# Optimization experiments

Hardware: AMD Instinct MI355X
Metric: run time of the kernel (lower is better)

The kernel has to match this reference:

```python
import jax, jax.numpy as jnp
import numpy as np

B = 4096
NUM_PTS = 1000

def de_boor(knotss, t, CP, p):
    # knotss: [N, K], t: [T, N], CP: [N, ncp, 2, 1] -> [T, N, 2, 1]
    N = knotss.shape[0]
    # k[b] = number of knots in knotss[b, p+1:] strictly below t (matches torch loop)
    k = jnp.sum((t[:, :, None] > knotss[None, :, p + 1:]).astype(jnp.int32), axis=-1)  # [T, N]
    bn = jnp.arange(N)[None, :, None]
    idx = k[:, :, None] + jnp.arange(p + 1)[None, None, :]           # [T, N, p+1]
    E = CP[bn, idx]                                                  # [T, N, p+1, 2, 1]
    te = t[:, :, None, None, None]
    for j in range(1, p + 1):
        m = p - j + 1
        i = jnp.arange(m)[None, None, :]
        a1 = knotss[bn, p + 1 + i + k[:, :, None]][..., None, None]  # [T, N, m, 1, 1]
        a2 = knotss[bn, i + j + k[:, :, None]][..., None, None]
        # in torch, ascending i reads old E[i+1]; vectorized update over old E is identical
        E = ((a1 - te) * E[:, :, :m] + (te - a2) * E[:, :, 1:m + 1]) / (a1 - a2)
    return E[:, :, 0]

def first_derivative(Pc, knots):
    n = Pc.shape[1]
    den = (knots[:, 4:n + 3] - knots[:, 1:n])[:, :, None, None]
    Q = 3.0 / den * (Pc[:, 1:] - Pc[:, :-1])
    return Q, knots[:, 1:-1]

def second_derivative(Q, knots):
    n = Q.shape[1]
    den = (knots[:, 3:n + 2] - knots[:, 1:n])[:, :, None, None]
    R = 2.0 / den * (Q[:, 1:] - Q[:, :-1])
    return R, knots[:, 1:-1]

def construct(t, knots, p=3):
    # t: [B], knots: [B, K] -> N: [B, K-1]; replicates stale-tail behavior of torch loop
    K = knots.shape[1]
    N = ((t[:, None] >= knots[:, :-1]) & (t[:, None] < knots[:, 1:])).astype(knots.dtype)
    lenN = K - 2
    for power in range(1, p + 1):
        m = lenN - power
        den_a = knots[:, power:power + m] - knots[:, :m]
        a = jnp.where(den_a != 0, (t[:, None] - knots[:, :m]) / jnp.where(den_a != 0, den_a, 1.0), 0.0)
        den_b = knots[:, power + 1:power + 1 + m] - knots[:, 1:1 + m]
        b = jnp.where(den_b != 0, (knots[:, power + 1:power + 1 + m] - t[:, None]) / jnp.where(den_b != 0, den_b, 1.0), 0.0)
        N = N.at[:, :m].set(N[:, :m] * a + N[:, 1:m + 1] * b)
    return N

def construct_A(knots):
    # knots: [B, 12], 6 data points -> A: [B, 8, 8]
    Bn = knots.shape[0]
    rows = [construct(knots[:, i + 3], knots) for i in range(5)]
    # i == 5 hits the knots[0, 8] == 1 branch (clamped right end): one-hot at column 7
    row5 = jnp.zeros((Bn, knots.shape[1] - 1), knots.dtype).at[:, 7].set(1.0)
    A = jnp.stack(rows + [row5], axis=1)[:, :, :8]                   # [B, 6, 8]
    z = jnp.zeros((Bn, 1, 8), knots.dtype)
    A = jnp.concatenate([z, A, z], axis=1)                           # [B, 8, 8]
    A = A.at[:, 0, 0].add(knots[:, 5]).at[:, 0, 1].add(-knots[:, 4] - knots[:, 5]).at[:, 0, 2].add(knots[:, 4])
    A = A.at[:, -1, -3].add(1.0 - knots[:, 7]).at[:, -1, -2].add(knots[:, 7] + knots[:, 6] - 2.0).at[:, -1, -1].add(1.0 - knots[:, 6])
    return A

def solve(P, knots):
    Bn = P.shape[0]
    z = jnp.zeros((Bn, 1, 1), P.dtype)
    Px = jnp.concatenate([z, P[:, :, 0], z], axis=1)  # [B, 8, 1]
    Py = jnp.concatenate([z, P[:, :, 1], z], axis=1)
    inv = jnp.linalg.inv(construct_A(knots))
    Cx = inv @ Px
    Cy = inv @ Py
    return jnp.concatenate([Cx, Cy], axis=2)[..., None]  # [B, 8, 2, 1]

def forward(x, P, W1, b1, W2, b2, W3, b3):
    h = jax.nn.relu(x @ W1.T + b1)
    h = jax.nn.relu(h @ W2.T + b2)
    xs = jax.nn.softmax(h @ W3.T + b3, axis=1)  # [B, 5]
    # torch: w[:, i] = x[:, i] + detach(w[:, i-1]) -> cumsum in value, identity in grad
    x4 = xs[:, :4]
    w = x4 + jax.lax.stop_gradient(jnp.cumsum(x4, axis=1) - x4)
    Bn = x.shape[0]
    knots = jnp.concatenate([jnp.zeros((Bn, 4), x.dtype), w, jnp.ones((Bn, 4), x.dtype)], axis=1)  # [B, 12]
    C = solve(P, knots)  # [B, 8, 2, 1]
    # global curvature over linspace(knots[0,3]=0, knots[0,10]=1, NUM_PTS)
    L = jnp.linspace(0.0, 1.0, NUM_PTS).astype(x.dtype)
    tall = jnp.broadcast_to(L[:, None], (NUM_PTS, Bn))
    Q, dk = first_derivative(C, knots)
    R, ddk = second_derivative(Q, dk)
    sp = de_boor(dk, tall, Q, 2)    # [T, B, 2, 1] spline'
    sdp = de_boor(ddk, tall, R, 1)  # [T, B, 2, 1] spline''
    spx, spy = sp[:, :, 0, 0], sp[:, :, 1, 0]
    sdx, sdy = sdp[:, :, 0, 0], sdp[:, :, 1, 0]
    speed2 = spx ** 2 + spy ** 2
    curv = (spx * sdy - spy * sdx) / (speed2 ** 3) ** 0.5
    vals = curv ** 2 * jnp.sqrt(speed2)  # [T, B]; de_boor(knots2, J, Q, 2) == spline', reused
    S1 = vals[1::2].sum(axis=0)
    S2 = vals[0::2].sum(axis=0)
    h_step = 1.0 / (NUM_PTS - 1)
    integration = h_step / 3.0 * (4.0 * S1 + 2.0 * S2)
    return integration, knots

def setup_inputs():
    key = jax.random.key(0)
    ks = jax.random.split(key, 8)
    return {
        "x": jax.random.normal(ks[0], (B, 8), jnp.float32),
        "P": jax.random.normal(ks[1], (B, 6, 2, 1), jnp.float32),
        "W1": jax.random.normal(ks[2], (128, 8), jnp.float32) * 0.3,
        "b1": jnp.full((128,), 0.01, jnp.float32),
        "W2": jax.random.normal(ks[3], (128, 128), jnp.float32) * 0.09,
        "b2": jnp.full((128,), 0.01, jnp.float32),
        "W3": jax.random.normal(ks[4], (5, 128), jnp.float32) * 0.1,
        "b3": jnp.full((5,), 0.01, jnp.float32),
    }

def reference(x, P, W1, b1, W2, b2, W3, b3):
    return forward(x, P, W1, b1, W2, b2, W3, b3)
```

## Files before the change

kernel.cpp:

```cpp
#include <hip/hip_runtime.h>
#include <math.h>

#define BATCH 4096
#define NPTS 1000

#define WSYNC() do { asm volatile("s_waitcnt lgkmcnt(0)" ::: "memory"); \
                     __builtin_amdgcn_sched_barrier(0); } while (0)

__device__ __forceinline__ float frcp(float v) { return __builtin_amdgcn_rcpf(v); }

__global__ __launch_bounds__(256, 8) void net2_one(
    const float* __restrict__ x, const float* __restrict__ P,
    const float* __restrict__ W1, const float* __restrict__ b1,
    const float* __restrict__ W2, const float* __restrict__ b2,
    const float* __restrict__ W3, const float* __restrict__ b3,
    float* __restrict__ out_integ, float* __restrict__ out_knots)
{
    __shared__ float s_h1[8][128];
    __shared__ float s_part[4][4][5];
    __shared__ float LA[8][8][10];
    __shared__ float LQ[8][16];
    __shared__ float LR[8][16];
    __shared__ float s_coef[8][64];

    const int tid = threadIdx.x;
    const int wv = tid >> 6, lane = tid & 63;
    const int p = tid >> 7, row = tid & 127;
    const int b0 = blockIdx.x * 8;

    {
        float4 w0 = ((const float4*)(W1 + row * 8))[0];
        float4 w1 = ((const float4*)(W1 + row * 8))[1];
        float bb = b1[row];
        #pragma unroll
        for (int k = 0; k < 4; ++k) {
            const float* xr = x + (b0 + p * 4 + k) * 8;
            float4 xa = ((const float4*)xr)[0];
            float4 xb = ((const float4*)xr)[1];
            float h = bb + w0.x*xa.x + w0.y*xa.y + w0.z*xa.z + w0.w*xa.w
                         + w1.x*xb.x + w1.y*xb.y + w1.z*xb.z + w1.w*xb.w;
            s_h1[p * 4 + k][row] = fmaxf(h, 0.f);
        }
    }
    __syncthreads();

    float bb2 = b2[row];
    float a0 = bb2, a1 = bb2, a2 = bb2, a3 = bb2;
    {
        const float4* wr = (const float4*)(W2 + row * 128);
        const float4* h0 = (const float4*)s_h1[p * 4 + 0];
        const float4* h1 = (const float4*)s_h1[p * 4 + 1];
        const float4* h2p = (const float4*)s_h1[p * 4 + 2];
        const float4* h3 = (const float4*)s_h1[p * 4 + 3];
        #pragma unroll 8
        for (int c4 = 0; c4 < 32; ++c4) {
            float4 w = wr[c4];
            float4 ha = h0[c4], hb = h1[c4], hc = h2p[c4], hd = h3[c4];
            a0 += w.x*ha.x + w.y*ha.y + w.z*ha.z + w.w*ha.w;
            a1 += w.x*hb.x + w.y*hb.y + w.z*hb.z + w.w*hb.w;
            a2 += w.x*hc.x + w.y*hc.y + w.z*hc.z + w.w*hc.w;
            a3 += w.x*hd.x + w.y*hd.y + w.z*hd.z + w.w*hd.w;
        }
    }
    float h2_0 = fmaxf(a0, 0.f), h2_1 = fmaxf(a1, 0.f);
    float h2_2 = fmaxf(a2, 0.f), h2_3 = fmaxf(a3, 0.f);

    #pragma unroll
    for (int c = 0; c < 5; ++c) {
        float wc = W3[c * 128 + row];
        float p0 = wc * h2_0, p1 = wc * h2_1, p2 = wc * h2_2, p3 = wc * h2_3;
        #pragma unroll
        for (int m = 32; m >= 1; m >>= 1) {
            p0 += __shfl_xor(p0, m, 64);
            p1 += __shfl_xor(p1, m, 64);
            p2 += __shfl_xor(p2, m, 64);
            p3 += __shfl_xor(p3, m, 64);
        }
        if (lane == 0) {
            s_part[wv][0][c] = p0; s_part[wv][1][c] = p1;
            s_part[wv][2][c] = p2; s_part[wv][3][c] = p3;
        }
    }
    __syncthreads();

    if (wv == 0) {
        const int el = lane >> 3, r = lane & 7;
        const int e = b0 + el;
        const int pw = (el >> 2) * 2;

        float lg0 = s_part[pw][el & 3][0] + s_part[pw + 1][el & 3][0] + b3[0];
        float lg1 = s_part[pw][el & 3][1] + s_part[pw + 1][el & 3][1] + b3[1];
        float lg2 = s_part[pw][el & 3][2] + s_part[pw + 1][el & 3][2] + b3[2];
        float lg3 = s_part[pw][el & 3][3] + s_part[pw + 1][el & 3][3] + b3[3];
        float lg4 = s_part[pw][el & 3][4] + s_part[pw + 1][el & 3][4] + b3[4];
        float mx = fmaxf(fmaxf(fmaxf(fmaxf(lg0, lg1), lg2), lg3), lg4);
        float e0 = expf(lg0-mx), e1 = expf(lg1-mx), e2 = expf(lg2-mx),
              e3 = expf(lg3-mx), e4 = expf(lg4-mx);
        float s = e0 + e1 + e2 + e3 + e4;
        float xs0 = e0/s, xs1 = e1/s, xs2 = e2/s, xs3 = e3/s;
        float c0 = xs0, c1 = c0 + xs1, c2 = c1 + xs2, c3 = c2 + xs3;
        float w4 = xs0 + (c0 - xs0);
        float w5 = xs1 + (c1 - xs1);
        float w6 = xs2 + (c2 - xs2);
        float w7 = xs3 + (c3 - xs3);

        {
            float kv = (r < 4) ? 0.f : (r == 4 ? w4 : r == 5 ? w5 : r == 6 ? w6 : w7);
            out_knots[e * 12 + r] = kv;
            if (r < 4) {
                out_knots[e * 12 + 8 + r] = 1.f;
                s_coef[el][60 + r] = (r == 0 ? w4 : r == 1 ? w5 : r == 2 ? w6 : w7);
            }
        }

        const float ka[12] = {0.f,0.f,0.f,0.f,w4,w5,w6,w7,1.f,1.f,1.f,1.f};
        float t = (r == 2) ? w4 : (r == 3) ? w5 : (r == 4) ? w6 : (r == 5) ? w7 : 0.f;
        float N[11];
        #pragma unroll
        for (int i = 0; i < 11; ++i)
            N[i] = (t >= ka[i] && t < ka[i+1]) ? 1.f : 0.f;
        #pragma unroll
        for (int pq = 1; pq <= 3; ++pq) {
            #pragma unroll
            for (int i = 0; i < 10; ++i) {
                if (i < 10 - pq) {
                    float da = ka[i+pq] - ka[i];
                    float av = (da != 0.f) ? (t - ka[i]) * frcp(da) : 0.f;
                    float db = ka[i+pq+1] - ka[i+1];
                    float bv = (db != 0.f) ? (ka[i+pq+1] - t) * frcp(db) : 0.f;
                    N[i] = N[i] * av + N[i+1] * bv;
                }
            }
        }

        float a[10];
        #pragma unroll
        for (int c = 0; c < 8; ++c) {
            float v0 = (c==0) ? w5 : (c==1) ? (-w4-w5) : (c==2) ? w4 : 0.f;
            float v6 = (c==7) ? 1.f : 0.f;
            float v7 = (c==5) ? (1.f-w7) : (c==6) ? (w7+w6-2.f) : (c==7) ? (1.f-w6) : 0.f;
            float vb = (r==0) ? v0 : (r==6) ? v6 : v7;
            a[c] = (r >= 1 && r <= 5) ? N[c] : vb;
        }
        {
            float px = 0.f, py = 0.f;
            if (r >= 1 && r <= 6) {
                px = P[e * 12 + (r-1) * 2 + 0];
                py = P[e * 12 + (r-1) * 2 + 1];
            }
            a[8] = px; a[9] = py;
        }

        int done = 0, pcol = 7;
        #pragma unroll
        for (int col = 0; col < 8; ++col) {
            float bv = done ? -1.f : fabsf(a[col]);
            int bi = lane;
            #pragma unroll
            for (int m = 1; m <= 4; m <<= 1) {
                float ov = __shfl_xor(bv, m, 64);
                int   oi = __shfl_xor(bi, m, 64);
                if (ov > bv || (ov == bv && oi < bi)) { bv = ov; bi = oi; }
            }
            float pr[10];
            #pragma unroll
            for (int c = 0; c < 10; ++c) pr[c] = __shfl(a[c], bi, 64);
            if (lane == bi) { done = 1; pcol = col; }
            else if (!done) {
                float f = a[col] * frcp(pr[col]);
                #pragma unroll
                for (int c = 0; c < 10; ++c) if (c > col) a[c] -= f * pr[c];
            }
        }
        #pragma unroll
        for (int c = 0; c < 10; ++c) LA[el][pcol][c] = a[c];
        WSYNC();

        if (r < 2) {
            const int par = r;
            float C[8];
            #pragma unroll
            for (int col = 7; col >= 0; --col) {
                float sv = LA[el][col][8 + par];
                #pragma unroll
                for (int c = col + 1; c < 8; ++c) sv -= LA[el][col][c] * C[c];
                C[col] = sv * frcp(LA[el][col][col]);
            }
            float Qr[7], Rr[6];
            const float dq[7] = { w4, w5, w6, w7 - w4, 1.f - w5, 1.f - w6, 1.f - w7 };
            #pragma unroll
            for (int i = 0; i < 7; ++i) Qr[i] = (3.f * frcp(dq[i])) * (C[i+1] - C[i]);
            const float dr[6] = { w4, w5, w6 - w4, w7 - w5, 1.f - w6, 1.f - w7 };
            #pragma unroll
            for (int i = 0; i < 6; ++i) Rr[i] = (2.f * frcp(dr[i])) * (Qr[i+1] - Qr[i]);
            #pragma unroll
            for (int i = 0; i < 7; ++i) LQ[el][i*2+par] = Qr[i];
            #pragma unroll
            for (int i = 0; i < 6; ++i) LR[el][i*2+par] = Rr[i];
        }
        WSYNC();

        if (r < 5) {
            const int s5 = r;
            float k2 = (s5 <= 1) ? 0.f : (s5 == 2) ? w4 : (s5 == 3) ? w5 : w6;
            float k3 = (s5 == 0) ? 0.f : (s5 == 1) ? w4 : (s5 == 2) ? w5 : (s5 == 3) ? w6 : w7;
            float k4 = (s5 == 0) ? w4 : (s5 == 1) ? w5 : (s5 == 2) ? w6 : (s5 == 3) ? w7 : 1.f;
            float k5 = (s5 == 0) ? w5 : (s5 == 1) ? w6 : (s5 == 2) ? w7 : 1.f;
            float q0x = LQ[el][s5*2],     q0y = LQ[el][s5*2+1];
            float q1x = LQ[el][(s5+1)*2], q1y = LQ[el][(s5+1)*2+1];
            float q2x = LQ[el][(s5+2)*2], q2y = LQ[el][(s5+2)*2+1];
            float r0x = LR[el][s5*2],     r0y = LR[el][s5*2+1];
            float r1x = LR[el][(s5+1)*2], r1y = LR[el][(s5+1)*2+1];
            float r42 = frcp(k4-k2), r53 = frcp(k5-k3), r43 = frcp(k4-k3);
            float A0x = (k4*q0x - k2*q1x)*r42, B0x = (q1x-q0x)*r42;
            float A1x = (k5*q1x - k3*q2x)*r53, B1x = (q2x-q1x)*r53;
            float c0x = r43*(k4*A0x - k3*A1x);
            float c1x = r43*(k4*B0x - A0x + A1x - k3*B1x);
            float c2x = r43*(B1x - B0x);
            float e0x = r43*(k4*r0x - k3*r1x);
            float e1x = r43*(r1x - r0x);
            float A0y = (k4*q0y - k2*q1y)*r42, B0y = (q1y-q0y)*r42;
            float A1y = (k5*q1y - k3*q2y)*r53, B1y = (q2y-q1y)*r53;
            float c0y = r43*(k4*A0y - k3*A1y);
            float c1y = r43*(k4*B0y - A0y + A1y - k3*B1y);
            float c2y = r43*(B1y - B0y);
            float e0y = r43*(k4*r0y - k3*r1y);
            float e1y = r43*(r1y - r0y);
            float* cb = &s_coef[el][s5 * 12];
            cb[0] = c0x; cb[1] = c1x; cb[2]  = c2x; cb[3]  = c0y;
            cb[4] = c1y; cb[5] = c2y; cb[6]  = e0x; cb[7]  = e1x;
            cb[8] = e0y; cb[9] = e1y; cb[10] = 0.f; cb[11] = 0.f;
        }
    }
    __syncthreads();

    const float c999 = 1.f / 999.f;
    #pragma unroll
    for (int q = 0; q < 2; ++q) {
        const int el = wv * 2 + q;
        const int e = b0 + el;
        float v = s_coef[el][lane];
        int vi = __float_as_int(v);
        float w4 = __int_as_float(__builtin_amdgcn_readlane(vi, 60));
        float w5 = __int_as_float(__builtin_amdgcn_readlane(vi, 61));
        float w6 = __int_as_float(__builtin_amdgcn_readlane(vi, 62));
        float w7 = __int_as_float(__builtin_amdgcn_readlane(vi, 63));

        auto bsearch = [&](float w) {
            int lo = 0, hi = 1000;
            #pragma unroll
            for (int it = 0; it < 10; ++it) {
                int mid = (lo + hi) >> 1;
                bool pr = ((float)mid * c999 > w);
                hi = pr ? mid : hi;
                lo = pr ? lo : (mid + 1);
            }
            return lo;
        };
        int B0 = bsearch(w4), B1 = bsearch(w5), B2 = bsearch(w6), B3 = bsearch(w7);

        float acc = 0.f;
        #define DOSEG(S, LOE, HIE) { \
            float cx0 = __int_as_float(__builtin_amdgcn_readlane(vi, (S)*12+0)); \
            float cx1 = __int_as_float(__builtin_amdgcn_readlane(vi, (S)*12+1)); \
            float cx2 = __int_as_float(__builtin_amdgcn_readlane(vi, (S)*12+2)); \
            float cy0 = __int_as_float(__builtin_amdgcn_readlane(vi, (S)*12+3)); \
            float cy1 = __int_as_float(__builtin_amdgcn_readlane(vi, (S)*12+4)); \
            float cy2 = __int_as_float(__builtin_amdgcn_readlane(vi, (S)*12+5)); \
            float ex0 = __int_as_float(__builtin_amdgcn_readlane(vi, (S)*12+6)); \
            float ex1 = __int_as_float(__builtin_amdgcn_readlane(vi, (S)*12+7)); \
            float ey0 = __int_as_float(__builtin_amdgcn_readlane(vi, (S)*12+8)); \
            float ey1 = __int_as_float(__builtin_amdgcn_readlane(vi, (S)*12+9)); \
            int lo = (LOE), hi = (HIE); \
            float wl = ((lo + lane) & 1) ? 4.f : 2.f; \
            for (int idx = lo + lane; idx < hi; idx += 64) { \
                float tt = (float)idx * c999; \
                float spx = (cx2 * tt + cx1) * tt + cx0; \
                float spy = (cy2 * tt + cy1) * tt + cy0; \
                float sdx = ex1 * tt + ex0; \
                float sdy = ey1 * tt + ey0; \
                float s2 = spx * spx + spy * spy; \
                float cross = spx * sdy - spy * sdx; \
                float rs = rsqrtf(s2); \
                float rs2 = rs * rs; \
                acc += wl * (cross * cross * (rs2 * rs2 * rs)); \
            } }
        DOSEG(0, 0,  B0)
        DOSEG(1, B0, B1)
        DOSEG(2, B1, B2)
        DOSEG(3, B2, B3)
        DOSEG(4, B3, 1000)
        #undef DOSEG

        #pragma unroll
        for (int m = 32; m >= 1; m >>= 1) acc += __shfl_xor(acc, m, 64);
        if (lane == 0) out_integ[e] = (1.f / 999.f) / 3.f * acc;
    }
}

extern "C" void kernel_launch(void* const* d_in, const int* in_sizes, int n_in,
                              void* d_out, int out_size, void* d_ws, size_t ws_size,
                              hipStream_t stream) {
    const float* x  = (const float*)d_in[0];
    const float* P  = (const float*)d_in[1];
    const float* W1 = (const float*)d_in[2];
    const float* b1 = (const float*)d_in[3];
    const float* W2 = (const float*)d_in[4];
    const float* b2 = (const float*)d_in[5];
    const float* W3 = (const float*)d_in[6];
    const float* b3 = (const float*)d_in[7];
    float* out_integ = (float*)d_out;
    float* out_knots = out_integ + BATCH;

    net2_one<<<dim3(BATCH / 8), dim3(256), 0, stream>>>(
        x, P, W1, b1, W2, b2, W3, b3, out_integ, out_knots);
}
```

Before: 28.84 us.

## Process two batch elements per block and split the integration across waves

Each block now handles 2 batch elements instead of 8, so the grid grows fourfold to 2048 blocks. Each wave integrates half of the 1000 sample points of one element, and the partial sums are combined through shared memory. The aim is more parallelism and shorter per-wave serial loops, keeping more CUs busy on MI355X. The cost is that W1/W2 weight loads are amortized over fewer elements per block, the MLP phase reuses data less, and the 16-thread serial solve phase is repeated in more blocks.

Measured after the change: 45.42 us. 57.5% more time.

```diff
diff --git a/kernel.cpp b/kernel.cpp
--- a/kernel.cpp
+++ b/kernel.cpp
@@ -16,83 +16,64 @@
     const float* __restrict__ W3, const float* __restrict__ b3,
     float* __restrict__ out_integ, float* __restrict__ out_knots)
 {
-    __shared__ float s_h1[8][128];
-    __shared__ float s_part[4][4][5];
-    __shared__ float LA[8][8][10];
-    __shared__ float LQ[8][16];
-    __shared__ float LR[8][16];
-    __shared__ float s_coef[8][64];
+    __shared__ float s_h1[2][128];
+    __shared__ float s_part[4][5];
+    __shared__ float LA[2][8][10];
+    __shared__ float LQ[2][16];
+    __shared__ float LR[2][16];
+    __shared__ float s_coef[2][64];
+    __shared__ float s_p[4];
 
     const int tid = threadIdx.x;
     const int wv = tid >> 6, lane = tid & 63;
-    const int p = tid >> 7, row = tid & 127;
-    const int b0 = blockIdx.x * 8;
+    const int elem = tid >> 7, row = tid & 127;
+    const int b0 = blockIdx.x * 2;
 
     {
         float4 w0 = ((const float4*)(W1 + row * 8))[0];
         float4 w1 = ((const float4*)(W1 + row * 8))[1];
-        float bb = b1[row];
-        #pragma unroll
-        for (int k = 0; k < 4; ++k) {
-            const float* xr = x + (b0 + p * 4 + k) * 8;
-            float4 xa = ((const float4*)xr)[0];
-            float4 xb = ((const float4*)xr)[1];
-            float h = bb + w0.x*xa.x + w0.y*xa.y + w0.z*xa.z + w0.w*xa.w
-                         + w1.x*xb.x + w1.y*xb.y + w1.z*xb.z + w1.w*xb.w;
-            s_h1[p * 4 + k][row] = fmaxf(h, 0.f);
-        }
+        const float* xr = x + (b0 + elem) * 8;
+        float4 xa = ((const float4*)xr)[0];
+        float4 xb = ((const float4*)xr)[1];
+        float h = b1[row] + w0.x*xa.x + w0.y*xa.y + w0.z*xa.z + w0.w*xa.w
+                          + w1.x*xb.x + w1.y*xb.y + w1.z*xb.z + w1.w*xb.w;
+        s_h1[elem][row] = fmaxf(h, 0.f);
     }
     __syncthreads();
 
-    float bb2 = b2[row];
-    float a0 = bb2, a1 = bb2, a2 = bb2, a3 = bb2;
+    float h2;
     {
+        float accA = b2[row], accB = 0.f;
         const float4* wr = (const float4*)(W2 + row * 128);
-        const float4* h0 = (const float4*)s_h1[p * 4 + 0];
-        const float4* h1 = (const float4*)s_h1[p * 4 + 1];
-        const float4* h2p = (const float4*)s_h1[p * 4 + 2];
-        const float4* h3 = (const float4*)s_h1[p * 4 + 3];
+        const float4* hh = (const float4*)s_h1[elem];
         #pragma unroll 8
-        for (int c4 = 0; c4 < 32; ++c4) {
-            float4 w = wr[c4];
-            float4 ha = h0[c4], hb = h1[c4], hc = h2p[c4], hd = h3[c4];
-            a0 += w.x*ha.x + w.y*ha.y + w.z*ha.z + w.w*ha.w;
-            a1 += w.x*hb.x + w.y*hb.y + w.z*hb.z + w.w*hb.w;
-            a2 += w.x*hc.x + w.y*hc.y + w.z*hc.z + w.w*hc.w;
-            a3 += w.x*hd.x + w.y*hd.y + w.z*hd.z + w.w*hd.w;
-        }
-    }
-    float h2_0 = fmaxf(a0, 0.f), h2_1 = fmaxf(a1, 0.f);
-    float h2_2 = fmaxf(a2, 0.f), h2_3 = fmaxf(a3, 0.f);
+        for (int c4 = 0; c4 < 32; c4 += 2) {
+            float4 wa = wr[c4],     ha = hh[c4];
+            float4 wb = wr[c4 + 1], hb = hh[c4 + 1];
+            accA += wa.x*ha.x + wa.y*ha.y + wa.z*ha.z + wa.w*ha.w;
+            accB += wb.x*hb.x + wb.y*hb.y + wb.z*hb.z + wb.w*hb.w;
+        }
+        h2 = fmaxf(accA + accB, 0.f);
+    }
 
     #pragma unroll
     for (int c = 0; c < 5; ++c) {
-        float wc = W3[c * 128 + row];
-        float p0 = wc * h2_0, p1 = wc * h2_1, p2 = wc * h2_2, p3 = wc * h2_3;
-        #pragma unroll
-        for (int m = 32; m >= 1; m >>= 1) {
-            p0 += __shfl_xor(p0, m, 64);
-            p1 += __shfl_xor(p1, m, 64);
-            p2 += __shfl_xor(p2, m, 64);
-            p3 += __shfl_xor(p3, m, 64);
-        }
-        if (lane == 0) {
-            s_part[wv][0][c] = p0; s_part[wv][1][c] = p1;
-            s_part[wv][2][c] = p2; s_part[wv][3][c] = p3;
-        }
+        float p = W3[c * 128 + row] * h2;
+        #pragma unroll
+        for (int m = 32; m >= 1; m >>= 1) p += __shfl_xor(p, m, 64);
+        if (lane == 0) s_part[wv][c] = p;
     }
     __syncthreads();
 
-    if (wv == 0) {
-        const int el = lane >> 3, r = lane & 7;
+    if (tid < 16) {
+        const int el = tid >> 3, r = tid & 7;
         const int e = b0 + el;
-        const int pw = (el >> 2) * 2;
-
-        float lg0 = s_part[pw][el & 3][0] + s_part[pw + 1][el & 3][0] + b3[0];
-        float lg1 = s_part[pw][el & 3][1] + s_part[pw + 1][el & 3][1] + b3[1];
-        float lg2 = s_part[pw][el & 3][2] + s_part[pw + 1][el & 3][2] + b3[2];
-        float lg3 = s_part[pw][el & 3][3] + s_part[pw + 1][el & 3][3] + b3[3];
-        float lg4 = s_part[pw][el & 3][4] + s_part[pw + 1][el & 3][4] + b3[4];
+
+        float lg0 = s_part[2*el][0] + s_part[2*el+1][0] + b3[0];
+        float lg1 = s_part[2*el][1] + s_part[2*el+1][1] + b3[1];
+        float lg2 = s_part[2*el][2] + s_part[2*el+1][2] + b3[2];
+        float lg3 = s_part[2*el][3] + s_part[2*el+1][3] + b3[3];
+        float lg4 = s_part[2*el][4] + s_part[2*el+1][4] + b3[4];
         float mx = fmaxf(fmaxf(fmaxf(fmaxf(lg0, lg1), lg2), lg3), lg4);
         float e0 = expf(lg0-mx), e1 = expf(lg1-mx), e2 = expf(lg2-mx),
               e3 = expf(lg3-mx), e4 = expf(lg4-mx);
@@ -155,7 +136,7 @@
         #pragma unroll
         for (int col = 0; col < 8; ++col) {
             float bv = done ? -1.f : fabsf(a[col]);
-            int bi = lane;
+            int bi = tid;
             #pragma unroll
             for (int m = 1; m <= 4; m <<= 1) {
                 float ov = __shfl_xor(bv, m, 64);
@@ -165,7 +146,7 @@
             float pr[10];
             #pragma unroll
             for (int c = 0; c < 10; ++c) pr[c] = __shfl(a[c], bi, 64);
-            if (lane == bi) { done = 1; pcol = col; }
+            if (tid == bi) { done = 1; pcol = col; }
             else if (!done) {
                 float f = a[col] * frcp(pr[col]);
                 #pragma unroll
@@ -234,11 +215,10 @@
     }
     __syncthreads();
 
-    const float c999 = 1.f / 999.f;
-    #pragma unroll
-    for (int q = 0; q < 2; ++q) {
-        const int el = wv * 2 + q;
-        const int e = b0 + el;
+    {
+        const int el = wv >> 1, half = wv & 1;
+        const int hlo = half * 500, hhi = hlo + 500;
+        const float c999 = 1.f / 999.f;
         float v = s_coef[el][lane];
         int vi = __float_as_int(v);
         float w4 = __int_as_float(__builtin_amdgcn_readlane(vi, 60));
@@ -261,6 +241,9 @@
 
         float acc = 0.f;
         #define DOSEG(S, LOE, HIE) { \
+            int lo = (LOE), hi = (HIE); \
+            lo = (lo > hlo) ? lo : hlo; \
+            hi = (hi < hhi) ? hi : hhi; \
             float cx0 = __int_as_float(__builtin_amdgcn_readlane(vi, (S)*12+0)); \
             float cx1 = __int_as_float(__builtin_amdgcn_readlane(vi, (S)*12+1)); \
             float cx2 = __int_as_float(__builtin_amdgcn_readlane(vi, (S)*12+2)); \
@@ -271,7 +254,6 @@
             float ex1 = __int_as_float(__builtin_amdgcn_readlane(vi, (S)*12+7)); \
             float ey0 = __int_as_float(__builtin_amdgcn_readlane(vi, (S)*12+8)); \
             float ey1 = __int_as_float(__builtin_amdgcn_readlane(vi, (S)*12+9)); \
-            int lo = (LOE), hi = (HIE); \
             float wl = ((lo + lane) & 1) ? 4.f : 2.f; \
             for (int idx = lo + lane; idx < hi; idx += 64) { \
                 float tt = (float)idx * c999; \
@@ -294,8 +276,11 @@
 
         #pragma unroll
         for (int m = 32; m >= 1; m >>= 1) acc += __shfl_xor(acc, m, 64);
-        if (lane == 0) out_integ[e] = (1.f / 999.f) / 3.f * acc;
-    }
+        if (lane == 0) s_p[wv] = acc;
+    }
+    __syncthreads();
+    if (tid < 2)
+        out_integ[b0 + tid] = (1.f / 999.f) / 3.f * (s_p[2 * tid] + s_p[2 * tid + 1]);
 }
 
 extern "C" void kernel_launch(void* const* d_in, const int* in_sizes, int n_in,
@@ -312,6 +297,6 @@
     float* out_integ = (float*)d_out;
     float* out_knots = out_integ + BATCH;
 
-    net2_one<<<dim3(BATCH / 8), dim3(256), 0, stream>>>(
+    net2_one<<<dim3(BATCH / 2), dim3(256), 0, stream>>>(
         x, P, W1, b1, W2, b2, W3, b3, out_integ, out_knots);
 }
```
